# Kernel optimization log

Hardware: AMD Instinct MI355X
Metric: run time of the kernel (lower is better)

Reference implementation:

```python
import jax, jax.numpy as jnp
import numpy as np

H = 1024        # pegasus-large hidden size
HEADS = 16      # matches the hard-coded /16 in the source
T = 512         # decoder steps
N = 1024        # encoder (source) tokens
V = 96103       # pegasus tokenizer vocab size


def setup_inputs() -> dict:
    key = jax.random.key(0)
    ks = jax.random.split(key, 8)
    return {
        "cross_attn": jax.random.normal(ks[0], (1, HEADS, T, N), jnp.float32),
        "encoder_hidden": jax.random.normal(ks[1], (1, N, H), jnp.float32),
        "decoder_hidden": jax.random.normal(ks[2], (1, T, H), jnp.float32),
        "decoder_embedding": jax.random.normal(ks[3], (1, T, H), jnp.float32),
        "logits": jax.random.normal(ks[4], (1, T, V), jnp.float32),
        "input_ids": jax.random.randint(ks[5], (N,), 0, V),
        "pointer_w": jax.random.normal(ks[6], (1, 3 * H), jnp.float32) * 0.02,
        "pointer_b": jnp.zeros((1,), jnp.float32),
    }


def reference(cross_attn, encoder_hidden, decoder_hidden, decoder_embedding,
              logits, input_ids, pointer_w, pointer_b):
    # squeeze batch dim (module assumes batch=1)
    ca = jnp.sum(cross_attn[0], axis=0) / 16.0                 # [T, N] head-avg cross attn
    enc = encoder_hidden[0]                                    # [N, H]
    dec_h = decoder_hidden[0]                                  # [T, H]
    dec_e = decoder_embedding[0]                               # [T, H]
    lg = logits[0]                                             # [T, V]

    h = ca @ enc                                               # [T, H] attn-weighted context
    lin = jnp.concatenate([h, dec_h, dec_e], axis=1)           # [T, 3H]
    gen_probs = jax.nn.sigmoid(lin @ pointer_w.T + pointer_b)  # [T, 1]

    distribution = jax.nn.softmax(lg, axis=1)                  # [T, V]
    gen_logits = gen_probs * distribution                      # [T, V]

    # vectorized form of: for t, for n: copy_logits[t, input_ids[n]] = ca[t, n]
    Tn, Vn = lg.shape
    rows = jnp.broadcast_to(jnp.arange(Tn)[:, None], ca.shape)       # [T, N]
    cols = jnp.broadcast_to(input_ids[None, :], ca.shape)            # [T, N]
    copy_logits = jnp.zeros((Tn, Vn), lg.dtype).at[rows, cols].set(ca)

    final_probs = gen_logits + (1.0 - gen_probs) * copy_logits  # [T, V]
    return gen_probs, final_probs
```

## Files before the change

### kernel.cpp

```cpp
#include <hip/hip_runtime.h>

#define Tn 512
#define Nn 1024
#define Hn 1024
#define Vn 96103u
#define NHEADS 16

typedef float f4 __attribute__((ext_vector_type(4)));

__device__ __forceinline__ unsigned enc1(float x) {
  unsigned u = __float_as_uint(x);
  u = u + 0x80000u + ((u >> 20) & 1u);
  return (u >> 20) - 896u;
}
__device__ __forceinline__ float dec1(unsigned w, int k) {
  unsigned byte = (w >> (8 * k)) & 0xFFu;
  return __uint_as_float((byte + 896u) << 20);
}

__global__ __launch_bounds__(256) void k0(const float* __restrict__ enc,
                                          const float* __restrict__ w,
                                          const int* __restrict__ ids,
                                          float* __restrict__ ew,
                                          int* __restrict__ col2n) {
  const int b = blockIdx.x, tid = threadIdx.x;
  if (b < Nn) {
    float4 r = ((const float4*)(enc + b * Hn))[tid];
    float4 ww = ((const float4*)w)[tid];
    float p = r.x * ww.x + r.y * ww.y + r.z * ww.z + r.w * ww.w;
    for (int off = 32; off > 0; off >>= 1) p += __shfl_down(p, off, 64);
    __shared__ float lds[4];
    int lane = tid & 63, wv = tid >> 6;
    if (lane == 0) lds[wv] = p;
    __syncthreads();
    if (tid == 0) ew[b] = lds[0] + lds[1] + lds[2] + lds[3];
    return;
  }
  for (int n = tid; n < (int)Nn; n += 256)
    atomicMax(&col2n[ids[n]], n);
}

__global__ __launch_bounds__(1024) void krow(
    const float* __restrict__ attn, const float* __restrict__ lg,
    const float* __restrict__ ew, const float* __restrict__ dh,
    const float* __restrict__ de, const float* __restrict__ w,
    const float* __restrict__ bias, const int* __restrict__ col2n,
    float* __restrict__ out) {
  __shared__ unsigned sm4[24064];
  __shared__ f4 accsh[4][256];
  __shared__ float cash[Nn];
  __shared__ float red[32];
  __shared__ float Pb[4];

  const int t = blockIdx.x, tid = threadIdx.x;
  const int lane = tid & 63, wv = tid >> 6;

  {
    const int g = tid >> 8, q = tid & 255;
    const f4* a4 = (const f4*)attn;
    f4 acc = __builtin_nontemporal_load(&a4[((unsigned)((g * 4) * Tn + t)) * 256u + q]);
#pragma unroll
    for (int k = 1; k < 4; ++k)
      acc += __builtin_nontemporal_load(&a4[((unsigned)((g * 4 + k) * Tn + t)) * 256u + q]);
    accsh[g][q] = acc;
  }
  __syncthreads();
  if (tid < 256) {
    f4 c = (accsh[0][tid] + accsh[1][tid] + accsh[2][tid] + accsh[3][tid]) * (1.0f / 16.0f);
    ((f4*)cash)[tid] = c;
  }
  __syncthreads();

  float gp = cash[tid] * ew[tid]
           + dh[t * Hn + tid] * w[Hn + tid]
           + de[t * Hn + tid] * w[2 * Hn + tid];

  const unsigned base = (unsigned)t * Vn;
  const unsigned end = base + Vn;
  const unsigned beg4 = (base + 3u) & ~3u;
  const unsigned end4 = end & ~3u;
  const unsigned q0 = beg4 / 4u;
  const unsigned nq = (end4 - beg4) / 4u;

  float s = 0.0f;
  for (unsigned i = base + tid; i < beg4; i += 1024)
    s += __expf(__builtin_nontemporal_load(&lg[i]));
  const f4* lg4 = (const f4*)lg;
  for (unsigned j = tid; j < nq; j += 1024) {
    f4 x = __builtin_nontemporal_load(&lg4[q0 + j]);
    float e0 = __expf(x[0]), e1 = __expf(x[1]), e2 = __expf(x[2]), e3 = __expf(x[3]);
    s += (e0 + e1) + (e2 + e3);
    sm4[j] = enc1(e0) | (enc1(e1) << 8) | (enc1(e2) << 16) | (enc1(e3) << 24);
  }
  for (unsigned i = end4 + tid; i < end; i += 1024)
    s += __expf(__builtin_nontemporal_load(&lg[i]));

  for (int off = 32; off > 0; off >>= 1) {
    gp += __shfl_down(gp, off, 64);
    s  += __shfl_down(s, off, 64);
  }
  if (lane == 0) { red[wv] = gp; red[16 + wv] = s; }
  __syncthreads();
  if (tid == 0) {
    float z = 0.f, S = 0.f;
#pragma unroll
    for (int q = 0; q < 16; ++q) { z += red[q]; S += red[16 + q]; }
    z += bias[0];
    float g = 1.0f / (1.0f + __expf(-z));
    out[t] = g;
    Pb[0] = g; Pb[1] = 1.0f / S; Pb[2] = 1.0f - g;
  }
  __syncthreads();

  const float g = Pb[0], inv = Pb[1], omg = Pb[2];
  float* outf = out + Tn;

  for (unsigned i = base + tid; i < beg4; i += 1024) {
    unsigned v = i - base;
    float val = g * __expf(__builtin_nontemporal_load(&lg[i])) * inv;
    int n = col2n[v];
    if (n >= 0) val += omg * cash[n];
    __builtin_nontemporal_store(val, &outf[i]);
  }
  f4* out4 = (f4*)outf;
  for (unsigned j = tid; j < nq; j += 1024) {
    unsigned dw = sm4[j];
    unsigned v = beg4 - base + 4u * j;
    f4 r;
    int n0 = col2n[v], n1 = col2n[v + 1], n2 = col2n[v + 2], n3 = col2n[v + 3];
    r[0] = g * dec1(dw, 0) * inv;
    r[1] = g * dec1(dw, 1) * inv;
    r[2] = g * dec1(dw, 2) * inv;
    r[3] = g * dec1(dw, 3) * inv;
    if (n0 >= 0) r[0] += omg * cash[n0];
    if (n1 >= 0) r[1] += omg * cash[n1];
    if (n2 >= 0) r[2] += omg * cash[n2];
    if (n3 >= 0) r[3] += omg * cash[n3];
    __builtin_nontemporal_store(r, &out4[q0 + j]);
  }
  for (unsigned i = end4 + tid; i < end; i += 1024) {
    unsigned v = i - base;
    float val = g * __expf(__builtin_nontemporal_load(&lg[i])) * inv;
    int n = col2n[v];
    if (n >= 0) val += omg * cash[n];
    __builtin_nontemporal_store(val, &outf[i]);
  }
}

extern "C" void kernel_launch(void* const* d_in, const int* in_sizes, int n_in,
                              void* d_out, int out_size, void* d_ws, size_t ws_size,
                              hipStream_t stream) {
  const float* attn = (const float*)d_in[0];
  const float* enc  = (const float*)d_in[1];
  const float* dh   = (const float*)d_in[2];
  const float* de   = (const float*)d_in[3];
  const float* lg   = (const float*)d_in[4];
  const int*   ids  = (const int*)d_in[5];
  const float* w    = (const float*)d_in[6];
  const float* b    = (const float*)d_in[7];
  float* out = (float*)d_out;

  float* ew    = (float*)d_ws;
  int*   col2n = (int*)(ew + Nn);

  hipMemsetAsync(col2n, 0xFF, (size_t)Vn * 4, stream);
  hipLaunchKernelGGL(k0, dim3(Nn + 1), dim3(256), 0, stream,
                     enc, w, ids, ew, col2n);
  hipLaunchKernelGGL(krow, dim3(Tn), dim3(1024), 0, stream,
                     attn, lg, ew, dh, de, w, b, col2n, out);
}
```

Baseline: 110.8 us.

## Shrink LDS exp cache with global spill and aligned column maps

Cuts the per-block LDS cache of packed exp values from 24064 to 18432 words and spills the remainder to a global workspace buffer. The aim is to fit two 1024-thread blocks per CU (launch bounds raised to 8). The column-to-token map is now built in four alignment-shifted copies so the main loop can fetch one int4 per quad instead of four scalar loads. The attention partial sums reuse the LDS cache buffer. The cost is extra global write/read traffic for the spilled tail and four times the atomic work in the map-building kernel.

```diff
diff --git a/kernel.cpp b/kernel.cpp
--- a/kernel.cpp
+++ b/kernel.cpp
@@ -5,6 +5,10 @@
 #define Hn 1024
 #define Vn 96103u
 #define NHEADS 16
+
+#define LQ 18432u
+#define TAILQ 5600u
+#define COLQN 24032u
 
 typedef float f4 __attribute__((ext_vector_type(4)));
 
@@ -22,7 +26,7 @@
                                           const float* __restrict__ w,
                                           const int* __restrict__ ids,
                                           float* __restrict__ ew,
-                                          int* __restrict__ col2n) {
+                                          int* __restrict__ colqI) {
   const int b = blockIdx.x, tid = threadIdx.x;
   if (b < Nn) {
     float4 r = ((const float4*)(enc + b * Hn))[tid];
@@ -36,18 +40,25 @@
     if (tid == 0) ew[b] = lds[0] + lds[1] + lds[2] + lds[3];
     return;
   }
-  for (int n = tid; n < (int)Nn; n += 256)
-    atomicMax(&col2n[ids[n]], n);
+  for (int n = tid; n < (int)Nn; n += 256) {
+    int c = ids[n];
+#pragma unroll
+    for (int r = 0; r < 4; ++r) {
+      int pos = c - r;
+      if (pos >= 0)
+        atomicMax(&colqI[((unsigned)r * COLQN + (unsigned)(pos >> 2)) * 4u +
+                         (unsigned)(pos & 3)], n);
+    }
+  }
 }
 
-__global__ __launch_bounds__(1024) void krow(
+__global__ __launch_bounds__(1024, 8) void krow(
     const float* __restrict__ attn, const float* __restrict__ lg,
     const float* __restrict__ ew, const float* __restrict__ dh,
     const float* __restrict__ de, const float* __restrict__ w,
-    const float* __restrict__ bias, const int* __restrict__ col2n,
-    float* __restrict__ out) {
-  __shared__ unsigned sm4[24064];
-  __shared__ f4 accsh[4][256];
+    const float* __restrict__ bias, const int4* __restrict__ colq4,
+    unsigned* __restrict__ ebuf4, float* __restrict__ out) {
+  __shared__ unsigned sm4[LQ];
   __shared__ float cash[Nn];
   __shared__ float red[32];
   __shared__ float Pb[4];
@@ -56,20 +67,22 @@
   const int lane = tid & 63, wv = tid >> 6;
 
   {
+    f4* accsh = (f4*)sm4;
     const int g = tid >> 8, q = tid & 255;
     const f4* a4 = (const f4*)attn;
     f4 acc = __builtin_nontemporal_load(&a4[((unsigned)((g * 4) * Tn + t)) * 256u + q]);
 #pragma unroll
     for (int k = 1; k < 4; ++k)
       acc += __builtin_nontemporal_load(&a4[((unsigned)((g * 4 + k) * Tn + t)) * 256u + q]);
-    accsh[g][q] = acc;
+    accsh[g * 256 + q] = acc;
+    __syncthreads();
+    if (tid < 256) {
+      f4 c = (accsh[tid] + accsh[256 + tid] + accsh[512 + tid] + accsh[768 + tid])
+             * (1.0f / 16.0f);
+      ((f4*)cash)[tid] = c;
+    }
+    __syncthreads();
   }
-  __syncthreads();
-  if (tid < 256) {
-    f4 c = (accsh[0][tid] + accsh[1][tid] + accsh[2][tid] + accsh[3][tid]) * (1.0f / 16.0f);
-    ((f4*)cash)[tid] = c;
-  }
-  __syncthreads();
 
   float gp = cash[tid] * ew[tid]
            + dh[t * Hn + tid] * w[Hn + tid]
@@ -81,6 +94,7 @@
   const unsigned end4 = end & ~3u;
   const unsigned q0 = beg4 / 4u;
   const unsigned nq = (end4 - beg4) / 4u;
+  const unsigned ebase = (unsigned)t * TAILQ;
 
   float s = 0.0f;
   for (unsigned i = base + tid; i < beg4; i += 1024)
@@ -90,7 +104,9 @@
     f4 x = __builtin_nontemporal_load(&lg4[q0 + j]);
     float e0 = __expf(x[0]), e1 = __expf(x[1]), e2 = __expf(x[2]), e3 = __expf(x[3]);
     s += (e0 + e1) + (e2 + e3);
-    sm4[j] = enc1(e0) | (enc1(e1) << 8) | (enc1(e2) << 16) | (enc1(e3) << 24);
+    unsigned dw = enc1(e0) | (enc1(e1) << 8) | (enc1(e2) << 16) | (enc1(e3) << 24);
+    if (j < LQ) sm4[j] = dw;
+    else        ebuf4[ebase + (j - LQ)] = dw;
   }
   for (unsigned i = end4 + tid; i < end; i += 1024)
     s += __expf(__builtin_nontemporal_load(&lg[i]));
@@ -114,34 +130,38 @@
 
   const float g = Pb[0], inv = Pb[1], omg = Pb[2];
   float* outf = out + Tn;
+  const int* colqI = (const int*)colq4;
 
   for (unsigned i = base + tid; i < beg4; i += 1024) {
     unsigned v = i - base;
     float val = g * __expf(__builtin_nontemporal_load(&lg[i])) * inv;
-    int n = col2n[v];
+    int n = colqI[(v >> 2) * 4u + (v & 3u)];
     if (n >= 0) val += omg * cash[n];
     __builtin_nontemporal_store(val, &outf[i]);
   }
-  f4* out4 = (f4*)outf;
-  for (unsigned j = tid; j < nq; j += 1024) {
-    unsigned dw = sm4[j];
-    unsigned v = beg4 - base + 4u * j;
-    f4 r;
-    int n0 = col2n[v], n1 = col2n[v + 1], n2 = col2n[v + 2], n3 = col2n[v + 3];
-    r[0] = g * dec1(dw, 0) * inv;
-    r[1] = g * dec1(dw, 1) * inv;
-    r[2] = g * dec1(dw, 2) * inv;
-    r[3] = g * dec1(dw, 3) * inv;
-    if (n0 >= 0) r[0] += omg * cash[n0];
-    if (n1 >= 0) r[1] += omg * cash[n1];
-    if (n2 >= 0) r[2] += omg * cash[n2];
-    if (n3 >= 0) r[3] += omg * cash[n3];
-    __builtin_nontemporal_store(r, &out4[q0 + j]);
+  {
+    const unsigned rt = (4u - (base & 3u)) & 3u;
+    const int4* cq = colq4 + rt * COLQN;
+    f4* out4 = (f4*)outf;
+    for (unsigned j = tid; j < nq; j += 1024) {
+      unsigned dw = (j < LQ) ? sm4[j] : ebuf4[ebase + (j - LQ)];
+      int4 nn = cq[j];
+      f4 r;
+      r[0] = g * dec1(dw, 0) * inv;
+      r[1] = g * dec1(dw, 1) * inv;
+      r[2] = g * dec1(dw, 2) * inv;
+      r[3] = g * dec1(dw, 3) * inv;
+      if (nn.x >= 0) r[0] += omg * cash[nn.x];
+      if (nn.y >= 0) r[1] += omg * cash[nn.y];
+      if (nn.z >= 0) r[2] += omg * cash[nn.z];
+      if (nn.w >= 0) r[3] += omg * cash[nn.w];
+      __builtin_nontemporal_store(r, &out4[q0 + j]);
+    }
   }
   for (unsigned i = end4 + tid; i < end; i += 1024) {
     unsigned v = i - base;
     float val = g * __expf(__builtin_nontemporal_load(&lg[i])) * inv;
-    int n = col2n[v];
+    int n = colqI[(v >> 2) * 4u + (v & 3u)];
     if (n >= 0) val += omg * cash[n];
     __builtin_nontemporal_store(val, &outf[i]);
   }
@@ -160,12 +180,13 @@
   const float* b    = (const float*)d_in[7];
   float* out = (float*)d_out;
 
-  float* ew    = (float*)d_ws;
-  int*   col2n = (int*)(ew + Nn);
+  int4*     colq4 = (int4*)d_ws;
+  unsigned* ebuf4 = (unsigned*)(colq4 + 4 * COLQN);
+  float*    ew    = (float*)(ebuf4 + (size_t)Tn * TAILQ);
 
-  hipMemsetAsync(col2n, 0xFF, (size_t)Vn * 4, stream);
+  hipMemsetAsync(colq4, 0xFF, (size_t)4 * COLQN * 16, stream);
   hipLaunchKernelGGL(k0, dim3(Nn + 1), dim3(256), 0, stream,
-                     enc, w, ids, ew, col2n);
+                     enc, w, ids, ew, (int*)colq4);
   hipLaunchKernelGGL(krow, dim3(Tn), dim3(1024), 0, stream,
-                     attn, lg, ew, dh, de, w, b, col2n, out);
+                     attn, lg, ew, dh, de, w, b, colq4, ebuf4, out);
 }
```

Measured after the change: 110.4 us. No clear change (-0.3%).
